# Optimization experiments

Measured on AMD Instinct MI355X. Metric: run time of the kernel, lower is better.

The kernel has to match this reference:

```python
import jax, jax.numpy as jnp
import numpy as np

N = 200000
B = 2
GX, GY, GZ = 480, 360, 32          # full-res voxel grid for input_coords
GX2, GY2, GZ2 = 240, 180, 16       # output_scale grid for bxyz_indx
CIN, CR, COUT = 64, 64, 64
CR2 = CR // 2
P_SCALE = (2, 4, 6, 8)


def setup_inputs() -> dict:
    key = jax.random.key(0)
    ks = jax.random.split(key, 24)
    s = 0.05
    input_data = jax.random.normal(ks[0], (N, CIN), dtype=jnp.float32)
    bcol = jax.random.randint(ks[1], (N, 1), 0, B, dtype=jnp.int32)
    xc = jax.random.randint(ks[2], (N, 1), 0, GX, dtype=jnp.int32)
    yc = jax.random.randint(ks[3], (N, 1), 0, GY, dtype=jnp.int32)
    zc = jax.random.randint(ks[4], (N, 1), 0, GZ, dtype=jnp.int32)
    input_coords = jnp.concatenate([bcol, xc, yc, zc], axis=1)
    input_coords_inv = jax.random.randint(ks[5], (N,), 0, N, dtype=jnp.int32)
    b2 = jax.random.randint(ks[6], (N, 1), 0, B, dtype=jnp.int32)
    x2 = jax.random.randint(ks[7], (N, 1), 0, GX2, dtype=jnp.int32)
    y2 = jax.random.randint(ks[8], (N, 1), 0, GY2, dtype=jnp.int32)
    z2 = jax.random.randint(ks[9], (N, 1), 0, GZ2, dtype=jnp.int32)
    bxyz_indx = jnp.concatenate([b2, x2, y2, z2], axis=1)
    # parameters (torch Linear stored here as [in, out])
    W_red = jax.random.normal(ks[10], (CIN, CR)) * s
    b_red = jnp.zeros((CR,), jnp.float32)
    fc_list_W = jax.random.normal(ks[11], (4, CR, CR2)) * s
    fc_list_b = jnp.zeros((4, CR2), jnp.float32)
    fcs_W = jax.random.normal(ks[12], (4, CR2, CR2)) * s
    fcs_b = jnp.zeros((4, CR2), jnp.float32)
    fc_W = jax.random.normal(ks[13], (CR2, CR2)) * s
    out_fc_W = jax.random.normal(ks[14], (CR2, CR)) * s
    lo_W1 = jax.random.normal(ks[15], (2 * CR, CR)) * s
    lo_W2 = jax.random.normal(ks[16], (CR, COUT)) * s
    lo_b2 = jnp.zeros((COUT,), jnp.float32)
    return dict(input_data=input_data, input_coords=input_coords,
                input_coords_inv=input_coords_inv, bxyz_indx=bxyz_indx,
                W_red=W_red, b_red=b_red, fc_list_W=fc_list_W, fc_list_b=fc_list_b,
                fcs_W=fcs_W, fcs_b=fcs_b, fc_W=fc_W, out_fc_W=out_fc_W,
                lo_W1=lo_W1, lo_W2=lo_W2, lo_b2=lo_b2)


def _segment_mean(x, seg, num_segments):
    sums = jax.ops.segment_sum(x, seg, num_segments=num_segments)
    cnt = jax.ops.segment_sum(jnp.ones((x.shape[0], 1), x.dtype), seg,
                              num_segments=num_segments)
    return sums / jnp.maximum(cnt, 1.0)


def reference(input_data, input_coords, input_coords_inv, bxyz_indx,
              W_red, b_red, fc_list_W, fc_list_b, fcs_W, fcs_b,
              fc_W, out_fc_W, lo_W1, lo_W2, lo_b2):
    reduced = jax.nn.relu(input_data @ W_red + b_red)          # [N, CR]
    bcol = input_coords[:, 0]
    xyz = input_coords[:, 1:]
    outs = []
    for j, ps in enumerate(P_SCALE):
        dx = (GX - 1) // ps + 1
        dy = (GY - 1) // ps + 1
        dz = (GZ - 1) // ps + 1
        q = xyz // ps                                          # [N, 3]
        # dense linearized voxel id replaces torch.unique(return_inverse)
        lin = ((bcol * dx + q[:, 0]) * dy + q[:, 1]) * dz + q[:, 2]
        nseg = B * dx * dy * dz
        fkm = _segment_mean(reduced, lin, nseg)                # [nseg, CR]
        att = jax.nn.relu(fkm @ fc_list_W[j] + fc_list_b[j])   # [nseg, CR2]
        outs.append(att[lin])                                  # gather back [N, CR2]
    scale_features = jnp.stack(outs, axis=1)                   # [N, 4, CR2]
    feat_S = scale_features.sum(axis=1)                        # [N, CR2]
    feat_Z = jax.nn.relu(feat_S @ fc_W)                        # [N, CR2]
    att_v = jax.nn.sigmoid(jnp.einsum('nc,kcd->nkd', feat_Z, fcs_W) + fcs_b)
    fused = (scale_features * att_v).sum(axis=1) @ out_fc_W    # [N, CR]
    output_f = jnp.concatenate([reduced, fused], axis=1)       # [N, 2*CR]
    proj = jax.nn.relu(output_f @ lo_W1) @ lo_W2 + lo_b2       # [N, COUT]
    proj = proj[input_coords_inv]
    # with_fm branch: index = (b, z, y, x) of bxyz_indx (b,x,y,z)
    lin2 = ((bxyz_indx[:, 0] * GZ2 + bxyz_indx[:, 3]) * GY2
            + bxyz_indx[:, 2]) * GX2 + bxyz_indx[:, 1]
    tv_fmap = jax.ops.segment_max(proj, lin2, num_segments=B * GZ2 * GY2 * GX2)
    tv_fmap = jnp.where(jnp.isneginf(tv_fmap), 0.0, tv_fmap)   # empty voxels -> 0
    return proj, tv_fmap, lin2
```

## Files before the change

kernel.cpp:

```cpp
#include <hip/hip_runtime.h>
#include <math.h>

#define NPTS   200000
#define CR     64
#define CR2    32

#define NSEG0      1382400
#define SUM123_ROW2 172800
#define SUM123_ROW3 230400
#define SUM123_ROWS 252000

#define TVSEG  1382400
#define GX2    240
#define GY2    180
#define GZ2    16

#define NBATCH 21600

__device__ __forceinline__ float bcastf(float v, int l) {
    return __int_as_float(__builtin_amdgcn_readlane(__float_as_int(v), l));
}

__device__ __forceinline__ int lin_scale(int b, int x, int y, int z,
                                         int ps, int dx, int dy, int dz) {
    int qx = x / ps, qy = y / ps, qz = z / ps;
    return ((b * dx + qx) * dy + qy) * dz + qz;
}

__device__ __forceinline__ void seg_decode(int seg, int& l1, int& l2, int& l3) {
    int qz = seg & 15; int rest = seg >> 4;
    int qy = rest % 180; int rest2 = rest / 180;
    int qx = rest2 % 240; int bb = rest2 / 240;
    l1 = ((bb * 120 + (qx >> 1)) * 90 + (qy >> 1)) * 8 + (qz >> 1);
    l2 = ((bb *  80 + (qx / 3)) * 60 + (qy / 3)) * 6 + (qz / 3);
    l3 = ((bb *  60 + (qx >> 2)) * 45 + (qy >> 2)) * 4 + (qz >> 2);
}

__device__ __forceinline__ int gatt_child(int s, int lane) {
    if (s < SUM123_ROW2) {
        int qz = s & 7, t = s >> 3;
        int qy = t % 90, t2 = t / 90;
        int qx = t2 % 120, b = t2 / 120;
        if (lane >= 8) return -1;
        int i = (lane >> 2) & 1, j = (lane >> 1) & 1, k = lane & 1;
        return ((b * 240 + 2 * qx + i) * 180 + 2 * qy + j) * 16 + 2 * qz + k;
    } else if (s < SUM123_ROW3) {
        int s2 = s - SUM123_ROW2;
        int qz = s2 % 6, t = s2 / 6;
        int qy = t % 60, t2 = t / 60;
        int qx = t2 % 80, b = t2 / 80;
        if (lane >= 27) return -1;
        int i = lane / 9, j = (lane / 3) % 3, k = lane % 3;
        int cz = 3 * qz + k;
        if (cz >= 16) return -1;
        return ((b * 240 + 3 * qx + i) * 180 + 3 * qy + j) * 16 + cz;
    } else {
        int s3 = s - SUM123_ROW3;
        int qz = s3 & 3, t = s3 >> 2;
        int qy = t % 45, t2 = t / 45;
        int qx = t2 % 60, b = t2 / 60;
        int i = lane >> 4, j = (lane >> 2) & 3, k = lane & 3;
        return ((b * 240 + 4 * qx + i) * 180 + 4 * qy + j) * 16 + 4 * qz + k;
    }
}

__global__ __launch_bounds__(256) void k_redscat(
        const float* __restrict__ in, const int* __restrict__ coords,
        const float* __restrict__ Wred, const float* __restrict__ bred,
        float* __restrict__ red, float* __restrict__ sum0,
        float* __restrict__ cnt) {
    __shared__ float Wl[CR * CR];
    for (int i = threadIdx.x; i < CR * CR; i += blockDim.x) Wl[i] = Wred[i];
    __syncthreads();
    int lane = threadIdx.x & 63;
    float bl = bred[lane];
    int wid  = blockIdx.x * 4 + (threadIdx.x >> 6);
    int nw   = gridDim.x * 4;
    for (int p = wid; p < NPTS / 2; p += nw) {
        int r0 = 2 * p, r1 = r0 + 1;
        float x0 = in[(size_t)r0 * CR + lane];
        float x1 = in[(size_t)r1 * CR + lane];
        float acc0 = bl, acc1 = bl;
#pragma unroll
        for (int k = 0; k < CR; ++k) {
            float w = Wl[k * CR + lane];
            acc0 += bcastf(x0, k) * w;
            acc1 += bcastf(x1, k) * w;
        }
        acc0 = fmaxf(acc0, 0.f); acc1 = fmaxf(acc1, 0.f);
        red[(size_t)r0 * CR + lane] = acc0;
        red[(size_t)r1 * CR + lane] = acc1;
        int4 c0 = ((const int4*)coords)[r0];
        int4 c1 = ((const int4*)coords)[r1];
        int l0a = lin_scale(c0.x, c0.y, c0.z, c0.w, 2, 240, 180, 16);
        int l0b = lin_scale(c1.x, c1.y, c1.z, c1.w, 2, 240, 180, 16);
        atomicAdd(&sum0[(size_t)l0a * CR + lane], acc0);
        atomicAdd(&sum0[(size_t)l0b * CR + lane], acc1);
        if (lane == 0) {
            atomicAdd(&cnt[l0a], 1.0f);
            atomicAdd(&cnt[l0b], 1.0f);
        }
    }
}

__global__ __launch_bounds__(256) void k_buildlist(
        const float* __restrict__ cnt, int* __restrict__ list0,
        int* __restrict__ listCount, int* __restrict__ rankArr,
        const float* __restrict__ outW, const float* __restrict__ loW1,
        float* __restrict__ M) {
    if (blockIdx.x >= 1080) {
        int e = (blockIdx.x - 1080) * 256 + threadIdx.x;
        if (e < 2048) {
            int r = e >> 6, c = e & 63;
            float acc = 0.f;
#pragma unroll
            for (int k = 0; k < 64; ++k)
                acc += outW[r * 64 + k] * loW1[(64 + k) * 64 + c];
            M[e] = acc;
        }
        return;
    }
    __shared__ int s_wavecnt[4];
    __shared__ int s_base;
    int lane = threadIdx.x & 63;
    int w = threadIdx.x >> 6;
    int batch0 = blockIdx.x * 20 + w * 5;
    int mycount = 0;
    for (int b = 0; b < 5; ++b) {
        float c = cnt[(batch0 + b) * 64 + lane];
        unsigned long long mask = __ballot(c > 0.f);
        mycount += __popcll(mask);
    }
    if (lane == 0) s_wavecnt[w] = mycount;
    __syncthreads();
    if (threadIdx.x == 0) {
        int tot = s_wavecnt[0] + s_wavecnt[1] + s_wavecnt[2] + s_wavecnt[3];
        s_base = atomicAdd(listCount, tot);
    }
    __syncthreads();
    int offset = s_base;
    for (int ww = 0; ww < w; ++ww) offset += s_wavecnt[ww];
    for (int b = 0; b < 5; ++b) {
        int cell = (batch0 + b) * 64 + lane;
        float c = cnt[cell];
        unsigned long long mask = __ballot(c > 0.f);
        if (c > 0.f) {
            int my = offset + __popcll(mask & ((1ull << lane) - 1ull));
            list0[my] = cell;
            rankArr[cell] = my;
        }
        offset += __popcll(mask);
    }
}

__global__ __launch_bounds__(256) void k_gatt(
        const float* __restrict__ sum0, float* __restrict__ attbuf,
        const float* __restrict__ cnt,
        const float* __restrict__ fcW, const float* __restrict__ fcB) {
    __shared__ float sw[3 * CR * CR2];
    for (int i = threadIdx.x; i < 3 * CR * CR2; i += blockDim.x)
        sw[i] = fcW[CR * CR2 + i];
    __syncthreads();
    int lane = threadIdx.x & 63;
    int d = lane & 31;
    int wid = blockIdx.x * 4 + (threadIdx.x >> 6);
    int nw  = gridDim.x * 4;
    for (int p = wid; p < SUM123_ROWS / 2; p += nw) {
        int s0 = 2 * p, s1 = s0 + 1;
        const float* w; float bj;
        if (s0 < SUM123_ROW2)      { w = sw;        bj = fcB[1 * CR2 + d]; }
        else if (s0 < SUM123_ROW3) { w = sw + 2048; bj = fcB[2 * CR2 + d]; }
        else                       { w = sw + 4096; bj = fcB[3 * CR2 + d]; }
        int cl0 = gatt_child(s0, lane);
        int cl1 = gatt_child(s1, lane);
        float c0 = (cl0 >= 0) ? cnt[cl0] : 0.f;
        float c1 = (cl1 >= 0) ? cnt[cl1] : 0.f;
        unsigned long long mask0 = __ballot(c0 > 0.f);
        unsigned long long mask1 = __ballot(c1 > 0.f);
        if (!(mask0 | mask1)) continue;
        float t0 = c0, t1 = c1;
#pragma unroll
        for (int sh = 1; sh <= 32; sh <<= 1) {
            t0 += __shfl_xor(t0, sh, 64);
            t1 += __shfl_xor(t1, sh, 64);
        }
        float acc0 = 0.f, acc1 = 0.f;
        while (mask0) {
            int j = __ffsll((long long)mask0) - 1; mask0 &= mask0 - 1;
            int cl = __builtin_amdgcn_readlane(cl0, j);
            acc0 += sum0[(size_t)cl * CR + lane];
        }
        while (mask1) {
            int j = __ffsll((long long)mask1) - 1; mask1 &= mask1 - 1;
            int cl = __builtin_amdgcn_readlane(cl1, j);
            acc1 += sum0[(size_t)cl * CR + lane];
        }
        float m0 = acc0 * (1.f / fmaxf(t0, 1.f));
        float m1 = acc1 * (1.f / fmaxf(t1, 1.f));
        float p0 = bj, p1 = bj;
#pragma unroll
        for (int k = 0; k < CR; ++k) {
            float wk = w[k * CR2 + d];
            p0 += bcastf(m0, k) * wk;
            p1 += bcastf(m1, k) * wk;
        }
        float a0 = fmaxf(p0, 0.f), a1 = fmaxf(p1, 0.f);
        if (lane < 32) attbuf[(size_t)s0 * CR2 + lane] = a0;
        else           attbuf[(size_t)s1 * CR2 + d]    = a1;
    }
}

__global__ __launch_bounds__(256) void k_segf(
        float* __restrict__ tv, const float* __restrict__ cnt,
        const int* __restrict__ list0, const int* __restrict__ listCount,
        const float* __restrict__ fcW, const float* __restrict__ fcB,
        const float* __restrict__ fc_W, const float* __restrict__ fcsW,
        const float* __restrict__ fcsB, const float* __restrict__ M,
        const float* __restrict__ attbuf, float* __restrict__ gc) {
    __shared__ float s_w0[2048];
    __shared__ float s_fcZ[1024];
    __shared__ float s_fcs[4096];
    __shared__ float s_M[2048];
    for (int i = threadIdx.x; i < 2048; i += 256) s_w0[i]  = fcW[i];
    for (int i = threadIdx.x; i < 1024; i += 256) s_fcZ[i] = fc_W[i];
    for (int i = threadIdx.x; i < 4096; i += 256) s_fcs[i] = fcsW[i];
    for (int i = threadIdx.x; i < 2048; i += 256) s_M[i]   = M[i];
    __syncthreads();

    int lane = threadIdx.x & 63;
    int d = lane & 31;
    int h = lane >> 5;
    float b0  = fcB[d];
    float vbA = fcsB[(h ? 1 : 0) * CR2 + d];
    float vbB = fcsB[(h ? 3 : 2) * CR2 + d];
    const float* VA = s_fcs + (h ? 1 : 0) * 1024;
    const float* VB = s_fcs + (h ? 3 : 2) * 1024;

    int total = listCount[0];
    int ngroups = (total + 3) >> 2;
    int wid = blockIdx.x * 4 + (threadIdx.x >> 6);
    int nw  = gridDim.x * 4;
    for (int g = wid; g < ngroups; g += nw) {
        int r0 = 4 * g;
        int r1 = min(r0 + 1, total - 1);
        int r2 = min(r0 + 2, total - 1);
        int r3 = min(r0 + 3, total - 1);
        int seg0 = list0[r0], seg1 = list0[r1], seg2 = list0[r2], seg3 = list0[r3];
        float* row0 = tv + (size_t)seg0 * CR;
        float* row1 = tv + (size_t)seg1 * CR;
        float* row2 = tv + (size_t)seg2 * CR;
        float* row3 = tv + (size_t)seg3 * CR;
        float m0 = row0[lane] * (1.f / cnt[seg0]);
        float m1 = row1[lane] * (1.f / cnt[seg1]);
        float m2 = row2[lane] * (1.f / cnt[seg2]);
        float m3 = row3[lane] * (1.f / cnt[seg3]);
        row0[lane] = 0.f; row1[lane] = 0.f; row2[lane] = 0.f; row3[lane] = 0.f;

        float p0 = b0, p1 = b0, p2 = b0, p3 = b0;
#pragma unroll
        for (int k = 0; k < CR; ++k) {
            float wk = s_w0[k * CR2 + d];
            p0 += bcastf(m0, k) * wk;
            p1 += bcastf(m1, k) * wk;
            p2 += bcastf(m2, k) * wk;
            p3 += bcastf(m3, k) * wk;
        }
        float a0_0 = fmaxf(p0, 0.f), a0_1 = fmaxf(p1, 0.f);
        float a0_2 = fmaxf(p2, 0.f), a0_3 = fmaxf(p3, 0.f);

        int l1_0, l2_0, l3_0, l1_1, l2_1, l3_1;
        int l1_2, l2_2, l3_2, l1_3, l2_3, l3_3;
        seg_decode(seg0, l1_0, l2_0, l3_0);
        seg_decode(seg1, l1_1, l2_1, l3_1);
        seg_decode(seg2, l1_2, l2_2, l3_2);
        seg_decode(seg3, l1_3, l2_3, l3_3);

        float a1_0 = attbuf[(size_t)l1_0 * CR2 + d];
        float a2_0 = attbuf[(size_t)(SUM123_ROW2 + l2_0) * CR2 + d];
        float a3_0 = attbuf[(size_t)(SUM123_ROW3 + l3_0) * CR2 + d];
        float a1_1 = attbuf[(size_t)l1_1 * CR2 + d];
        float a2_1 = attbuf[(size_t)(SUM123_ROW2 + l2_1) * CR2 + d];
        float a3_1 = attbuf[(size_t)(SUM123_ROW3 + l3_1) * CR2 + d];
        float a1_2 = attbuf[(size_t)l1_2 * CR2 + d];
        float a2_2 = attbuf[(size_t)(SUM123_ROW2 + l2_2) * CR2 + d];
        float a3_2 = attbuf[(size_t)(SUM123_ROW3 + l3_2) * CR2 + d];
        float a1_3 = attbuf[(size_t)l1_3 * CR2 + d];
        float a2_3 = attbuf[(size_t)(SUM123_ROW2 + l2_3) * CR2 + d];
        float a3_3 = attbuf[(size_t)(SUM123_ROW3 + l3_3) * CR2 + d];

        float fS0 = a0_0 + a1_0 + a2_0 + a3_0;
        float fS1 = a0_1 + a1_1 + a2_1 + a3_1;
        float fS2 = a0_2 + a1_2 + a2_2 + a3_2;
        float fS3 = a0_3 + a1_3 + a2_3 + a3_3;

        float z0 = 0.f, z1 = 0.f, z2 = 0.f, z3 = 0.f;
#pragma unroll
        for (int cc = 0; cc < CR2; ++cc) {
            float wz = s_fcZ[cc * CR2 + d];
            z0 += bcastf(fS0, cc) * wz;
            z1 += bcastf(fS1, cc) * wz;
            z2 += bcastf(fS2, cc) * wz;
            z3 += bcastf(fS3, cc) * wz;
        }
        float fZ0 = fmaxf(z0, 0.f), fZ1 = fmaxf(z1, 0.f);
        float fZ2 = fmaxf(z2, 0.f), fZ3 = fmaxf(z3, 0.f);

        float avA0 = vbA, avA1 = vbA, avA2 = vbA, avA3 = vbA;
        float avB0 = vbB, avB1 = vbB, avB2 = vbB, avB3 = vbB;
#pragma unroll
        for (int cc = 0; cc < CR2; ++cc) {
            float wa = VA[cc * CR2 + d];
            float wb = VB[cc * CR2 + d];
            float f0 = bcastf(fZ0, cc), f1 = bcastf(fZ1, cc);
            float f2 = bcastf(fZ2, cc), f3 = bcastf(fZ3, cc);
            avA0 += f0 * wa; avB0 += f0 * wb;
            avA1 += f1 * wa; avB1 += f1 * wb;
            avA2 += f2 * wa; avB2 += f2 * wb;
            avA3 += f3 * wa; avB3 += f3 * wb;
        }
        avA0 = 1.f / (1.f + __expf(-avA0)); avB0 = 1.f / (1.f + __expf(-avB0));
        avA1 = 1.f / (1.f + __expf(-avA1)); avB1 = 1.f / (1.f + __expf(-avB1));
        avA2 = 1.f / (1.f + __expf(-avA2)); avB2 = 1.f / (1.f + __expf(-avB2));
        avA3 = 1.f / (1.f + __expf(-avA3)); avB3 = 1.f / (1.f + __expf(-avB3));

        float u0 = (h ? a1_0 : a0_0) * avA0 + (h ? a3_0 : a2_0) * avB0;
        float u1 = (h ? a1_1 : a0_1) * avA1 + (h ? a3_1 : a2_1) * avB1;
        float u2 = (h ? a1_2 : a0_2) * avA2 + (h ? a3_2 : a2_2) * avB2;
        float u3 = (h ? a1_3 : a0_3) * avA3 + (h ? a3_3 : a2_3) * avB3;
        float fI0 = u0 + __shfl_xor(u0, 32, 64);
        float fI1 = u1 + __shfl_xor(u1, 32, 64);
        float fI2 = u2 + __shfl_xor(u2, 32, 64);
        float fI3 = u3 + __shfl_xor(u3, 32, 64);

        float g0 = 0.f, g1 = 0.f, g2 = 0.f, g3 = 0.f;
#pragma unroll
        for (int dd = 0; dd < CR2; ++dd) {
            float wm = s_M[dd * CR + lane];
            g0 += bcastf(fI0, dd) * wm;
            g1 += bcastf(fI1, dd) * wm;
            g2 += bcastf(fI2, dd) * wm;
            g3 += bcastf(fI3, dd) * wm;
        }
        gc[(size_t)r0 * CR + lane] = g0;
        gc[(size_t)r1 * CR + lane] = g1;
        gc[(size_t)r2 * CR + lane] = g2;
        gc[(size_t)r3 * CR + lane] = g3;
    }
}

__device__ __forceinline__ unsigned int fkey(float f) {
    unsigned int b = __float_as_uint(f);
    return (b & 0x80000000u) ? ~b : (b | 0x80000000u);
}

__global__ __launch_bounds__(256) void k_pgmax(
        const float* __restrict__ red, const float* __restrict__ gc,
        const int* __restrict__ rankArr,
        const int* __restrict__ coords, const int* __restrict__ inv,
        const int* __restrict__ bxyz,
        const float* __restrict__ loW1, const float* __restrict__ loW2,
        const float* __restrict__ lob2, float* __restrict__ outProj,
        float* __restrict__ outLin, unsigned int* __restrict__ tvKey,
        unsigned char* __restrict__ flags) {
    __shared__ float s_W1[4096];
    __shared__ float s_W2[4096];
    for (int i = threadIdx.x; i < 4096; i += 256) s_W1[i] = loW1[i];
    for (int i = threadIdx.x; i < 4096; i += 256) s_W2[i] = loW2[i];
    __syncthreads();

    int lane = threadIdx.x & 63;
    float lob = lob2[lane];
    int wid = blockIdx.x * 4 + (threadIdx.x >> 6);
    int nw  = gridDim.x * 4;
    for (int q = wid; q < NPTS / 4; q += nw) {
        int i0 = 4 * q, i1 = i0 + 1, i2 = i0 + 2, i3 = i0 + 3;
        int s0 = inv[i0], s1 = inv[i1], s2 = inv[i2], s3 = inv[i3];
        int4 c0 = ((const int4*)coords)[s0];
        int4 c1 = ((const int4*)coords)[s1];
        int4 c2 = ((const int4*)coords)[s2];
        int4 c3 = ((const int4*)coords)[s3];
        int l0 = lin_scale(c0.x, c0.y, c0.z, c0.w, 2, 240, 180, 16);
        int l1 = lin_scale(c1.x, c1.y, c1.z, c1.w, 2, 240, 180, 16);
        int l2 = lin_scale(c2.x, c2.y, c2.z, c2.w, 2, 240, 180, 16);
        int l3 = lin_scale(c3.x, c3.y, c3.z, c3.w, 2, 240, 180, 16);
        int rk0 = rankArr[l0], rk1 = rankArr[l1];
        int rk2 = rankArr[l2], rk3 = rankArr[l3];

        int4 b0 = ((const int4*)bxyz)[i0];
        int4 b1 = ((const int4*)bxyz)[i1];
        int4 b2 = ((const int4*)bxyz)[i2];
        int4 b3 = ((const int4*)bxyz)[i3];
        int n0 = ((b0.x * GZ2 + b0.w) * GY2 + b0.z) * GX2 + b0.y;
        int n1 = ((b1.x * GZ2 + b1.w) * GY2 + b1.z) * GX2 + b1.y;
        int n2 = ((b2.x * GZ2 + b2.w) * GY2 + b2.z) * GX2 + b2.y;
        int n3 = ((b3.x * GZ2 + b3.w) * GY2 + b3.z) * GX2 + b3.y;
        if (lane == 0) {
            outLin[i0] = (float)n0; flags[n0] = 1;
            outLin[i1] = (float)n1; flags[n1] = 1;
            outLin[i2] = (float)n2; flags[n2] = 1;
            outLin[i3] = (float)n3; flags[n3] = 1;
        }

        float x0 = red[(size_t)s0 * CR + lane];
        float x1 = red[(size_t)s1 * CR + lane];
        float x2 = red[(size_t)s2 * CR + lane];
        float x3 = red[(size_t)s3 * CR + lane];
        float h0 = gc[(size_t)rk0 * CR + lane];
        float h1 = gc[(size_t)rk1 * CR + lane];
        float h2 = gc[(size_t)rk2 * CR + lane];
        float h3 = gc[(size_t)rk3 * CR + lane];
#pragma unroll
        for (int k = 0; k < CR; ++k) {
            float w = s_W1[k * CR + lane];
            h0 += bcastf(x0, k) * w;
            h1 += bcastf(x1, k) * w;
            h2 += bcastf(x2, k) * w;
            h3 += bcastf(x3, k) * w;
        }
        h0 = fmaxf(h0, 0.f); h1 = fmaxf(h1, 0.f);
        h2 = fmaxf(h2, 0.f); h3 = fmaxf(h3, 0.f);

        float q0 = lob, q1 = lob, q2 = lob, q3 = lob;
#pragma unroll
        for (int k = 0; k < CR; ++k) {
            float w = s_W2[k * CR + lane];
            q0 += bcastf(h0, k) * w;
            q1 += bcastf(h1, k) * w;
            q2 += bcastf(h2, k) * w;
            q3 += bcastf(h3, k) * w;
        }
        outProj[(size_t)i0 * CR + lane] = q0;
        outProj[(size_t)i1 * CR + lane] = q1;
        outProj[(size_t)i2 * CR + lane] = q2;
        outProj[(size_t)i3 * CR + lane] = q3;

        atomicMax(&tvKey[(size_t)n0 * CR + lane], fkey(q0));
        atomicMax(&tvKey[(size_t)n1 * CR + lane], fkey(q1));
        atomicMax(&tvKey[(size_t)n2 * CR + lane], fkey(q2));
        atomicMax(&tvKey[(size_t)n3 * CR + lane], fkey(q3));
    }
}

__global__ __launch_bounds__(256) void k_fix(
        unsigned int* __restrict__ tv, const unsigned char* __restrict__ flags) {
    int lane = threadIdx.x & 63;
    int wid = blockIdx.x * 4 + (threadIdx.x >> 6);
    int nw  = gridDim.x * 4;
    for (int batch = wid; batch < NBATCH; batch += nw) {
        int base = batch * 64;
        unsigned char f = flags[base + lane];
        unsigned long long mask = __ballot(f != 0);
        while (mask) {
            int j = __ffsll((long long)mask) - 1; mask &= mask - 1;
            size_t idx = (size_t)(base + j) * CR + lane;
            unsigned int k = tv[idx];
            float v = (k == 0u) ? 0.f
                    : __uint_as_float((k & 0x80000000u) ? (k & 0x7FFFFFFFu) : ~k);
            ((float*)tv)[idx] = v;
        }
    }
}

extern "C" void kernel_launch(void* const* d_in, const int* in_sizes, int n_in,
                              void* d_out, int out_size, void* d_ws, size_t ws_size,
                              hipStream_t stream) {
    (void)in_sizes; (void)n_in; (void)out_size; (void)ws_size;
    const float* in_data = (const float*)d_in[0];
    const int*   coords  = (const int*)d_in[1];
    const int*   inv     = (const int*)d_in[2];
    const int*   bxyz    = (const int*)d_in[3];
    const float* W_red   = (const float*)d_in[4];
    const float* b_red   = (const float*)d_in[5];
    const float* fcW     = (const float*)d_in[6];
    const float* fcB     = (const float*)d_in[7];
    const float* fcsW    = (const float*)d_in[8];
    const float* fcsB    = (const float*)d_in[9];
    const float* fc_W    = (const float*)d_in[10];
    const float* outW    = (const float*)d_in[11];
    const float* loW1    = (const float*)d_in[12];
    const float* loW2    = (const float*)d_in[13];
    const float* lob2    = (const float*)d_in[14];

    float* outProj = (float*)d_out;
    float* tv      = outProj + (size_t)NPTS * CR;
    float* outLin  = tv + (size_t)TVSEG * CR;

    float* ws_f   = (float*)d_ws;
    float* red    = ws_f;
    float* attbuf = red + (size_t)NPTS * CR;
    float* cnt    = attbuf + (size_t)SUM123_ROWS * CR2;
    int*   listCount = (int*)(cnt + (size_t)NSEG0);
    unsigned char* flags = (unsigned char*)(listCount + 4);
    int*   rankArr   = (int*)(flags + (size_t)TVSEG);
    int*   list0     = rankArr + (size_t)NSEG0;
    float* gc     = (float*)(list0 + (size_t)NPTS);
    float* Mmat   = gc + (size_t)NPTS * CR;

    hipMemsetAsync(tv, 0, (size_t)TVSEG * CR * sizeof(float), stream);
    hipMemsetAsync(cnt, 0, (size_t)NSEG0 * 4 + 16 + (size_t)TVSEG, stream);

    k_redscat<<<2048, 256, 0, stream>>>(in_data, coords, W_red, b_red,
                                        red, tv, cnt);
    k_buildlist<<<1088, 256, 0, stream>>>(cnt, list0, listCount, rankArr,
                                          outW, loW1, Mmat);
    k_gatt<<<2048, 256, 0, stream>>>(tv, attbuf, cnt, fcW, fcB);
    k_segf<<<2048, 256, 0, stream>>>(tv, cnt, list0, (const int*)listCount,
                                     fcW, fcB, fc_W, fcsW, fcsB, Mmat,
                                     attbuf, gc);
    k_pgmax<<<2048, 256, 0, stream>>>(red, gc, rankArr, coords, inv, bxyz,
                                      loW1, loW2, lob2, outProj,
                                      outLin, (unsigned int*)tv, flags);
    k_fix<<<2048, 256, 0, stream>>>((unsigned int*)tv, flags);
}
```

Before: 1.028 ms.

## Merge list-building into coarse attention kernel and gather children densely

Folds the list-building and M-matrix blocks into the coarse-scale attention kernel, with disjoint block ranges for each role, so one launch replaces two. The per-cell child sum now loads every child voxel row at a fixed offset pattern with unrolled loops, instead of iterating a ballot mask over the non-empty children. This removes the serial readlane/ffs loop and lets the loads issue in parallel, but it also reads the zero-filled rows of empty children, which means far more memory traffic on sparse grids. Blocks that fill the shared weight array are now mixed with blocks that do not touch it.

```diff
diff --git a/kernel.cpp b/kernel.cpp
--- a/kernel.cpp
+++ b/kernel.cpp
@@ -103,13 +103,20 @@
     }
 }
 
-__global__ __launch_bounds__(256) void k_buildlist(
-        const float* __restrict__ cnt, int* __restrict__ list0,
-        int* __restrict__ listCount, int* __restrict__ rankArr,
+__global__ __launch_bounds__(256) void k_gatt(
+        const float* __restrict__ sum0, float* __restrict__ attbuf,
+        const float* __restrict__ cnt,
+        const float* __restrict__ fcW, const float* __restrict__ fcB,
+        int* __restrict__ list0, int* __restrict__ listCount,
+        int* __restrict__ rankArr,
         const float* __restrict__ outW, const float* __restrict__ loW1,
         float* __restrict__ M) {
-    if (blockIdx.x >= 1080) {
-        int e = (blockIdx.x - 1080) * 256 + threadIdx.x;
+    __shared__ float sw[3 * CR * CR2];
+    __shared__ int s_wavecnt[4];
+    __shared__ int s_base;
+
+    if (blockIdx.x < 8) {
+        int e = blockIdx.x * 256 + threadIdx.x;
         if (e < 2048) {
             int r = e >> 6, c = e & 63;
             float acc = 0.f;
@@ -120,57 +127,53 @@
         }
         return;
     }
-    __shared__ int s_wavecnt[4];
-    __shared__ int s_base;
-    int lane = threadIdx.x & 63;
-    int w = threadIdx.x >> 6;
-    int batch0 = blockIdx.x * 20 + w * 5;
-    int mycount = 0;
-    for (int b = 0; b < 5; ++b) {
-        float c = cnt[(batch0 + b) * 64 + lane];
-        unsigned long long mask = __ballot(c > 0.f);
-        mycount += __popcll(mask);
-    }
-    if (lane == 0) s_wavecnt[w] = mycount;
-    __syncthreads();
-    if (threadIdx.x == 0) {
-        int tot = s_wavecnt[0] + s_wavecnt[1] + s_wavecnt[2] + s_wavecnt[3];
-        s_base = atomicAdd(listCount, tot);
-    }
-    __syncthreads();
-    int offset = s_base;
-    for (int ww = 0; ww < w; ++ww) offset += s_wavecnt[ww];
-    for (int b = 0; b < 5; ++b) {
-        int cell = (batch0 + b) * 64 + lane;
-        float c = cnt[cell];
-        unsigned long long mask = __ballot(c > 0.f);
-        if (c > 0.f) {
-            int my = offset + __popcll(mask & ((1ull << lane) - 1ull));
-            list0[my] = cell;
-            rankArr[cell] = my;
-        }
-        offset += __popcll(mask);
-    }
-}
-
-__global__ __launch_bounds__(256) void k_gatt(
-        const float* __restrict__ sum0, float* __restrict__ attbuf,
-        const float* __restrict__ cnt,
-        const float* __restrict__ fcW, const float* __restrict__ fcB) {
-    __shared__ float sw[3 * CR * CR2];
+    if (blockIdx.x < 1088) {
+        int lane = threadIdx.x & 63;
+        int w = threadIdx.x >> 6;
+        int batch0 = (blockIdx.x - 8) * 20 + w * 5;
+        int mycount = 0;
+        for (int b = 0; b < 5; ++b) {
+            float c = cnt[(batch0 + b) * 64 + lane];
+            unsigned long long mask = __ballot(c > 0.f);
+            mycount += __popcll(mask);
+        }
+        if (lane == 0) s_wavecnt[w] = mycount;
+        __syncthreads();
+        if (threadIdx.x == 0) {
+            int tot = s_wavecnt[0] + s_wavecnt[1] + s_wavecnt[2] + s_wavecnt[3];
+            s_base = atomicAdd(listCount, tot);
+        }
+        __syncthreads();
+        int offset = s_base;
+        for (int ww = 0; ww < w; ++ww) offset += s_wavecnt[ww];
+        for (int b = 0; b < 5; ++b) {
+            int cell = (batch0 + b) * 64 + lane;
+            float c = cnt[cell];
+            unsigned long long mask = __ballot(c > 0.f);
+            if (c > 0.f) {
+                int my = offset + __popcll(mask & ((1ull << lane) - 1ull));
+                list0[my] = cell;
+                rankArr[cell] = my;
+            }
+            offset += __popcll(mask);
+        }
+        return;
+    }
+
     for (int i = threadIdx.x; i < 3 * CR * CR2; i += blockDim.x)
         sw[i] = fcW[CR * CR2 + i];
     __syncthreads();
     int lane = threadIdx.x & 63;
     int d = lane & 31;
-    int wid = blockIdx.x * 4 + (threadIdx.x >> 6);
-    int nw  = gridDim.x * 4;
+    int wid = (blockIdx.x - 1088) * 4 + (threadIdx.x >> 6);
+    int nw  = 2048 * 4;
     for (int p = wid; p < SUM123_ROWS / 2; p += nw) {
         int s0 = 2 * p, s1 = s0 + 1;
         const float* w; float bj;
         if (s0 < SUM123_ROW2)      { w = sw;        bj = fcB[1 * CR2 + d]; }
         else if (s0 < SUM123_ROW3) { w = sw + 2048; bj = fcB[2 * CR2 + d]; }
         else                       { w = sw + 4096; bj = fcB[3 * CR2 + d]; }
+
         int cl0 = gatt_child(s0, lane);
         int cl1 = gatt_child(s1, lane);
         float c0 = (cl0 >= 0) ? cnt[cl0] : 0.f;
@@ -184,17 +187,52 @@
             t0 += __shfl_xor(t0, sh, 64);
             t1 += __shfl_xor(t1, sh, 64);
         }
+
         float acc0 = 0.f, acc1 = 0.f;
-        while (mask0) {
-            int j = __ffsll((long long)mask0) - 1; mask0 &= mask0 - 1;
-            int cl = __builtin_amdgcn_readlane(cl0, j);
-            acc0 += sum0[(size_t)cl * CR + lane];
-        }
-        while (mask1) {
-            int j = __ffsll((long long)mask1) - 1; mask1 &= mask1 - 1;
-            int cl = __builtin_amdgcn_readlane(cl1, j);
-            acc1 += sum0[(size_t)cl * CR + lane];
-        }
+        if (s0 < SUM123_ROW2) {
+            int qz = s0 & 7, t = s0 >> 3;
+            int qy = t % 90, t2 = t / 90;
+            int qx = t2 % 120, b = t2 / 120;
+            int base0 = ((b * 240 + 2 * qx) * 180 + 2 * qy) * 16 + 2 * qz;
+            int base1 = base0 + 2;
+#pragma unroll
+            for (int c = 0; c < 8; ++c) {
+                int off = (c >> 2) * 2880 + ((c >> 1) & 1) * 16 + (c & 1);
+                acc0 += sum0[(size_t)(base0 + off) * CR + lane];
+                acc1 += sum0[(size_t)(base1 + off) * CR + lane];
+            }
+        } else if (s0 < SUM123_ROW3) {
+            int s2 = s0 - SUM123_ROW2;
+            int qz = s2 % 6, t = s2 / 6;
+            int qy = t % 60, t2 = t / 60;
+            int qx = t2 % 80, b = t2 / 80;
+            int base0 = ((b * 240 + 3 * qx) * 180 + 3 * qy) * 16 + 3 * qz;
+            int base1 = base0 + 3;
+            int kmax1 = (qz == 4) ? 1 : 3;
+#pragma unroll
+            for (int ij = 0; ij < 9; ++ij) {
+                int rb = (ij / 3) * 2880 + (ij % 3) * 16;
+#pragma unroll
+                for (int k = 0; k < 3; ++k)
+                    acc0 += sum0[(size_t)(base0 + rb + k) * CR + lane];
+                for (int k = 0; k < kmax1; ++k)
+                    acc1 += sum0[(size_t)(base1 + rb + k) * CR + lane];
+            }
+        } else {
+            int s3 = s0 - SUM123_ROW3;
+            int qz = s3 & 3, t = s3 >> 2;
+            int qy = t % 45, t2 = t / 45;
+            int qx = t2 % 60, b = t2 / 60;
+            int base0 = ((b * 240 + 4 * qx) * 180 + 4 * qy) * 16 + 4 * qz;
+            int base1 = base0 + 4;
+#pragma unroll
+            for (int c = 0; c < 64; ++c) {
+                int off = (c >> 4) * 2880 + ((c >> 2) & 3) * 16 + (c & 3);
+                acc0 += sum0[(size_t)(base0 + off) * CR + lane];
+                acc1 += sum0[(size_t)(base1 + off) * CR + lane];
+            }
+        }
+
         float m0 = acc0 * (1.f / fmaxf(t0, 1.f));
         float m1 = acc1 * (1.f / fmaxf(t1, 1.f));
         float p0 = bj, p1 = bj;
@@ -501,9 +539,9 @@
 
     k_redscat<<<2048, 256, 0, stream>>>(in_data, coords, W_red, b_red,
                                         red, tv, cnt);
-    k_buildlist<<<1088, 256, 0, stream>>>(cnt, list0, listCount, rankArr,
-                                          outW, loW1, Mmat);
-    k_gatt<<<2048, 256, 0, stream>>>(tv, attbuf, cnt, fcW, fcB);
+    k_gatt<<<3136, 256, 0, stream>>>(tv, attbuf, cnt, fcW, fcB,
+                                     list0, listCount, rankArr,
+                                     outW, loW1, Mmat);
     k_segf<<<2048, 256, 0, stream>>>(tv, cnt, list0, (const int*)listCount,
                                      fcW, fcB, fc_W, fcsW, fcsB, Mmat,
                                      attbuf, gc);
```

Measured after the change: 1.118 ms. +8.7%, slower.
